# Kernel optimization log

Measured on AMD Instinct MI355X. Metric: run time of the kernel, lower is better.

Reference implementation:

```python
import jax, jax.numpy as jnp
import numpy as np

N = 100000
E = 1600000
IN_C = 128
OUT_C = 64
HID = 2 * OUT_C  # 128


def gcn_conv(x, src, dst, W, b, n):
    # PyG GCNConv with add_self_loops=True, symmetric normalization, bias.
    h = x @ W  # [n, d_out] - transform first (PyG order)
    ones = jnp.ones(src.shape[0], dtype=h.dtype)
    deg = jax.ops.segment_sum(ones, dst, num_segments=n)  # includes self-loops -> deg >= 1
    dinv = jax.lax.rsqrt(deg)
    norm = dinv[src] * dinv[dst]  # [E+n]
    msg = h[src] * norm[:, None]  # gather + scale
    return jax.ops.segment_sum(msg, dst, num_segments=n) + b


def setup_inputs() -> dict:
    key = jax.random.key(0)
    ks = jax.random.split(key, 8)
    x = jax.random.normal(ks[0], (N, IN_C), dtype=jnp.float32)
    edge_index = jax.random.randint(ks[1], (2, E), 0, N, dtype=jnp.int64)
    s1 = 1.0 / np.sqrt(IN_C)
    s2 = 1.0 / np.sqrt(HID)
    s3 = 1.0 / np.sqrt(OUT_C)
    W1 = jax.random.normal(ks[2], (IN_C, HID), dtype=jnp.float32) * s1
    b1 = jnp.zeros((HID,), dtype=jnp.float32)
    W2 = jax.random.normal(ks[3], (HID, OUT_C), dtype=jnp.float32) * s2
    b2 = jnp.zeros((OUT_C,), dtype=jnp.float32)
    Wfc = jax.random.normal(ks[4], (OUT_C, OUT_C), dtype=jnp.float32) * s3
    bfc = jax.random.uniform(ks[5], (OUT_C,), dtype=jnp.float32, minval=-s3, maxval=s3)
    return {"x": x, "edge_index": edge_index, "W1": W1, "b1": b1,
            "W2": W2, "b2": b2, "Wfc": Wfc, "bfc": bfc}


def reference(x, edge_index, W1, b1, W2, b2, Wfc, bfc):
    n = x.shape[0]
    loop = jnp.arange(n, dtype=edge_index.dtype)
    src = jnp.concatenate([edge_index[0], loop])  # add self-loops
    dst = jnp.concatenate([edge_index[1], loop])
    h = jax.nn.relu(gcn_conv(x, src, dst, W1, b1, n))
    h = gcn_conv(h, src, dst, W2, b2, n)
    return h @ Wfc + bfc
```

## Files before the change

### kernel.cpp

```cpp
#include <hip/hip_runtime.h>

#define INC  128
#define HIDC 128
#define OUTC 64

#define BSH   8
#define NBMAX 512
#define HB    128
#define TILE  4096
#define CAP   8192

typedef unsigned int  u32;
typedef unsigned short u16;
typedef short bf16x8 __attribute__((ext_vector_type(8)));
typedef float f32x4 __attribute__((ext_vector_type(4)));

static __device__ __forceinline__ u16 f2bf(float f) {
    u32 u = __builtin_bit_cast(u32, f);
    u += 0x7fffu + ((u >> 16) & 1u);
    return (u16)(u >> 16);
}
static __device__ __forceinline__ float bf_lo(u32 u) {
    return __builtin_bit_cast(float, u << 16);
}
static __device__ __forceinline__ float bf_hi(u32 u) {
    return __builtin_bit_cast(float, u & 0xffff0000u);
}


__global__ __launch_bounds__(256) void bhist_kernel(const int* __restrict__ dst,
                                                    int* __restrict__ parts,
                                                    int E, int nb) {
    __shared__ int h[NBMAX];
    for (int i = threadIdx.x; i < NBMAX; i += 256) h[i] = 0;
    __syncthreads();
    const int total = HB * 256;
    for (int e = blockIdx.x * 256 + threadIdx.x; e < E; e += total)
        atomicAdd(&h[dst[e] >> BSH], 1);
    __syncthreads();
    for (int i = threadIdx.x; i < nb; i += 256) parts[i * HB + blockIdx.x] = h[i];
}

__global__ __launch_bounds__(512) void bscan_kernel(const int* __restrict__ parts,
                                                    int* __restrict__ bucketOff, int nb) {
    __shared__ int sums[NBMAX];
    const int tid = threadIdx.x;
    int s = 0;
    if (tid < nb) {
        const int* p = parts + tid * HB;
#pragma unroll 8
        for (int r = 0; r < HB; ++r) s += p[r];
    }
    sums[tid] = s;
    __syncthreads();
    for (int d = 1; d < NBMAX; d <<= 1) {
        int t = sums[tid];
        int a = (tid >= d) ? sums[tid - d] : 0;
        __syncthreads();
        sums[tid] = t + a;
        __syncthreads();
    }
    if (tid < nb) bucketOff[tid] = sums[tid] - s;
    if (tid == NBMAX - 1) bucketOff[nb] = sums[NBMAX - 1];
}

__global__ __launch_bounds__(256) void multisplit_kernel(const int* __restrict__ src,
                                                         const int* __restrict__ dst,
                                                         const int* __restrict__ bucketOff,
                                                         int* __restrict__ gfill,
                                                         u32* __restrict__ binned,
                                                         int E, int nb) {
    __shared__ int hist[NBMAX];
    __shared__ int sbase[NBMAX];
    __shared__ int cursor[NBMAX];
    __shared__ int gposs[NBMAX];
    __shared__ int wsum[4];
    __shared__ int2 buf[TILE];
    const int tid  = threadIdx.x;
    const int base = blockIdx.x * TILE;
    const int cnt  = min(TILE, E - base);

    for (int i = tid; i < NBMAX; i += 256) hist[i] = 0;
    __syncthreads();

    int ls[16], ld[16], dg[16];
#pragma unroll
    for (int k = 0; k < 16; ++k) {
        int idx = tid + k * 256;
        if (idx < cnt) {
            ls[k] = src[base + idx];
            ld[k] = dst[base + idx];
            dg[k] = ld[k] >> BSH;
            atomicAdd(&hist[dg[k]], 1);
        } else dg[k] = -1;
    }
    __syncthreads();
    {
        const int a = hist[2 * tid], b = hist[2 * tid + 1];
        const int s = a + b;
        const int lane = tid & 63;
        int incl = s;
#pragma unroll
        for (int d = 1; d < 64; d <<= 1) {
            int t = __shfl_up(incl, d);
            if (lane >= d) incl += t;
        }
        if (lane == 63) wsum[tid >> 6] = incl;
        __syncthreads();
        const int w = tid >> 6;
        int wbase = 0;
        if (w > 0) wbase += wsum[0];
        if (w > 1) wbase += wsum[1];
        if (w > 2) wbase += wsum[2];
        const int excl = wbase + incl - s;
        sbase[2 * tid] = excl;          cursor[2 * tid] = excl;
        sbase[2 * tid + 1] = excl + a;  cursor[2 * tid + 1] = excl + a;
    }
    __syncthreads();
#pragma unroll
    for (int k = 0; k < 16; ++k) {
        if (dg[k] >= 0) {
            int p = atomicAdd(&cursor[dg[k]], 1);
            buf[p] = make_int2(ls[k], ld[k]);
        }
    }
    __syncthreads();
    for (int d = tid; d < nb; d += 256) {
        int c = cursor[d] - sbase[d];
        gposs[d] = (c > 0) ? atomicAdd(&gfill[d], c) : 0;
    }
    __syncthreads();
    for (int idx = tid; idx < cnt; idx += 256) {
        int2 e = buf[idx];
        int d = e.y >> BSH;
        binned[bucketOff[d] + gposs[d] + (idx - sbase[d])] =
            (u32)e.x | ((u32)(e.y & 255) << 24);
    }
}

__global__ __launch_bounds__(256) void csr_build_kernel(const u32* __restrict__ binned,
                                                        const int* __restrict__ bucketOff,
                                                        int* __restrict__ col,
                                                        int* __restrict__ rowptr,
                                                        float* __restrict__ dinv,
                                                        int n, int E) {
    __shared__ int cnt[257];
    __shared__ int excl[256];
    __shared__ int wsum[4];
    __shared__ int colstage[CAP];
    const int tid   = threadIdx.x;
    const int b     = blockIdx.x;
    const int node0 = b << BSH;
    const int nNodes = min(256, n - node0);
    const int e0 = bucketOff[b], e1 = bucketOff[b + 1];
    const int ec = e1 - e0;

    for (int i = tid; i <= 256; i += 256) cnt[i] = 0;
    __syncthreads();
    for (int i = tid; i < ec; i += 256)
        atomicAdd(&cnt[binned[e0 + i] >> 24], 1);
    __syncthreads();
    const int myc = cnt[tid];
    {
        const int lane = tid & 63;
        int incl = myc;
#pragma unroll
        for (int d = 1; d < 64; d <<= 1) {
            int t = __shfl_up(incl, d);
            if (lane >= d) incl += t;
        }
        if (lane == 63) wsum[tid >> 6] = incl;
        __syncthreads();
        const int w = tid >> 6;
        int wbase = 0;
        if (w > 0) wbase += wsum[0];
        if (w > 1) wbase += wsum[1];
        if (w > 2) wbase += wsum[2];
        excl[tid] = wbase + incl - myc;
    }
    __syncthreads();
    if (tid < nNodes) {
        const int node = node0 + tid;
        rowptr[node] = e0 + excl[tid];
        dinv[node] = rsqrtf((float)(myc + 1));
    }
    if (b == 0 && tid == 0) rowptr[n] = E;
    __syncthreads();
    cnt[tid] = excl[tid];
    __syncthreads();
    if (ec <= CAP) {
        for (int i = tid; i < ec; i += 256) {
            u32 e = binned[e0 + i];
            int p = atomicAdd(&cnt[e >> 24], 1);
            colstage[p] = (int)(e & 0xffffffu);
        }
        __syncthreads();
        for (int i = tid; i < ec; i += 256) col[e0 + i] = colstage[i];
    } else {
        for (int i = tid; i < ec; i += 256) {
            u32 e = binned[e0 + i];
            int p = atomicAdd(&cnt[e >> 24], 1);
            col[e0 + p] = (int)(e & 0xffffffu);
        }
    }
}

__global__ __launch_bounds__(256) void fold_kernel(const float* __restrict__ W1,
                                                   const float* __restrict__ W2,
                                                   const float* __restrict__ Wfc,
                                                   const float* __restrict__ b2,
                                                   const float* __restrict__ bfc,
                                                   u16* __restrict__ W1t,
                                                   u16* __restrict__ W2ft,
                                                   float* __restrict__ b2f) {
    int t = blockIdx.x * 256 + threadIdx.x;
    if (t < HIDC * HIDC) {
        int nn = t >> 7, k = t & 127;
        W1t[nn * HIDC + k] = f2bf(W1[k * HIDC + nn]);
    } else if (t < HIDC * HIDC + HIDC * OUTC) {
        int u = t - HIDC * HIDC;
        int i = u >> 6, j = u & 63;
        float s = 0.f;
#pragma unroll 8
        for (int k = 0; k < OUTC; ++k) s = fmaf(W2[i * OUTC + k], Wfc[k * OUTC + j], s);
        W2ft[j * HIDC + i] = f2bf(s);
    } else if (t < HIDC * HIDC + HIDC * OUTC + OUTC) {
        int j = t - HIDC * HIDC - HIDC * OUTC;
        float s = bfc[j];
#pragma unroll 8
        for (int k = 0; k < OUTC; ++k) s = fmaf(b2[k], Wfc[k * OUTC + j], s);
        b2f[j] = s;
    }
}


template <int N, bool AF32>
__global__ __launch_bounds__(256) void mfma_gemm_kernel(const void* __restrict__ Aptr,
                                                        const u16* __restrict__ Wt,
                                                        const float* __restrict__ dinv,
                                                        u16* __restrict__ out, int M) {
    constexpr int K = 128;
    constexpr int NC = N / 16;
    __shared__ u16 Ws[N * K];

    const int tid = threadIdx.x;
    for (int id = tid; id < N * K / 8; id += 256) {
        int nn = id >> 4;
        int c  = id & 15;
        uint4 v = *(const uint4*)(Wt + nn * K + c * 8);
        int slot = (nn << 4) + (c ^ (nn & 7));
        *(uint4*)((char*)Ws + slot * 16) = v;
    }

    const int wave = tid >> 6;
    const int lane = tid & 63;
    const int r0   = blockIdx.x * 64 + wave * 16;
    const int arow = r0 + (lane & 15);
    const int kgrp = lane >> 4;
    __syncthreads();

    f32x4 acc[NC];
#pragma unroll
    for (int nc = 0; nc < NC; ++nc) acc[nc] = f32x4{0.f, 0.f, 0.f, 0.f};

#pragma unroll
    for (int kc = 0; kc < 4; ++kc) {
        bf16x8 af = {0, 0, 0, 0, 0, 0, 0, 0};
        if (arow < M) {
            if constexpr (AF32) {
                const float* ap = (const float*)Aptr + (size_t)arow * K + kc * 32 + kgrp * 8;
                float4 v0 = *(const float4*)ap;
                float4 v1 = *(const float4*)(ap + 4);
                af[0] = (short)f2bf(v0.x); af[1] = (short)f2bf(v0.y);
                af[2] = (short)f2bf(v0.z); af[3] = (short)f2bf(v0.w);
                af[4] = (short)f2bf(v1.x); af[5] = (short)f2bf(v1.y);
                af[6] = (short)f2bf(v1.z); af[7] = (short)f2bf(v1.w);
            } else {
                af = *(const bf16x8*)((const u16*)Aptr + (size_t)arow * K + kc * 32 + kgrp * 8);
            }
        }
#pragma unroll
        for (int nc = 0; nc < NC; ++nc) {
            int nn = nc * 16 + (lane & 15);
            int slot = (nn << 4) + ((kc * 4 + kgrp) ^ (nn & 7));
            bf16x8 bfr = *(const bf16x8*)((const char*)Ws + slot * 16);
            acc[nc] = __builtin_amdgcn_mfma_f32_16x16x32_bf16(af, bfr, acc[nc], 0, 0, 0);
        }
    }
#pragma unroll
    for (int reg = 0; reg < 4; ++reg) {
        int row = r0 + (lane >> 4) * 4 + reg;
        if (row <= M) {
            float sc = (row < M) ? dinv[row] : 0.f;
#pragma unroll
            for (int nc = 0; nc < NC; ++nc)
                out[(size_t)row * N + nc * 16 + (lane & 15)] = f2bf(acc[nc][reg] * sc);
        }
    }
}


__global__ __launch_bounds__(256) void agg1_kernel(const u16* __restrict__ g,
                                                   const int* __restrict__ rowptr,
                                                   const int* __restrict__ col,
                                                   const float* __restrict__ dinv,
                                                   const float* __restrict__ b1,
                                                   u32* __restrict__ h1, int n) {
    const int wid  = threadIdx.x >> 6;
    const int lane = threadIdx.x & 63;
    const int v = blockIdx.x * 4 + wid;
    if (v >= n) return;
    const int h = lane >> 5;
    const int r = lane & 31;
    const int base = rowptr[v], endi = rowptr[v + 1];

    float a0 = 0.f, a1 = 0.f, a2 = 0.f, a3 = 0.f;
    float b0 = 0.f, b1v = 0.f, b2v = 0.f, b3 = 0.f;
    {
        uint2 sv = *(const uint2*)(g + ((size_t)v << 7) + (r << 2));
        if (h == 0) {
            a0 = bf_lo(sv.x); a1 = bf_hi(sv.x);
            a2 = bf_lo(sv.y); a3 = bf_hi(sv.y);
        }
    }

    for (int c = base; c < endi; c += 64) {
        const int m = min(64, endi - c);
        const int idx = (lane < m) ? col[c + lane] : n;
        for (int i = 0; i < m; i += 8) {
            int u0 = __shfl(idx, i + h);
            int u1 = __shfl(idx, i + 2 + h);
            int u2 = __shfl(idx, i + 4 + h);
            int u3 = __shfl(idx, i + 6 + h);
            uint2 x0 = *(const uint2*)(g + ((size_t)u0 << 7) + (r << 2));
            uint2 x1 = *(const uint2*)(g + ((size_t)u1 << 7) + (r << 2));
            uint2 x2 = *(const uint2*)(g + ((size_t)u2 << 7) + (r << 2));
            uint2 x3 = *(const uint2*)(g + ((size_t)u3 << 7) + (r << 2));
            a0 += bf_lo(x0.x); a1 += bf_hi(x0.x); a2 += bf_lo(x0.y); a3 += bf_hi(x0.y);
            b0 += bf_lo(x1.x); b1v += bf_hi(x1.x); b2v += bf_lo(x1.y); b3 += bf_hi(x1.y);
            a0 += bf_lo(x2.x); a1 += bf_hi(x2.x); a2 += bf_lo(x2.y); a3 += bf_hi(x2.y);
            b0 += bf_lo(x3.x); b1v += bf_hi(x3.x); b2v += bf_lo(x3.y); b3 += bf_hi(x3.y);
        }
    }
    float s0 = a0 + b0, s1 = a1 + b1v, s2 = a2 + b2v, s3 = a3 + b3;
    s0 += __shfl_xor(s0, 32);
    s1 += __shfl_xor(s1, 32);
    s2 += __shfl_xor(s2, 32);
    s3 += __shfl_xor(s3, 32);
    if (h == 0) {
        const float dv = dinv[v];
        const float4 bb = *(const float4*)&b1[r << 2];
        float o0 = fmaxf(fmaf(dv, s0, bb.x), 0.f);
        float o1 = fmaxf(fmaf(dv, s1, bb.y), 0.f);
        float o2 = fmaxf(fmaf(dv, s2, bb.z), 0.f);
        float o3 = fmaxf(fmaf(dv, s3, bb.w), 0.f);
        uint2 pk;
        pk.x = (u32)f2bf(o0) | ((u32)f2bf(o1) << 16);
        pk.y = (u32)f2bf(o2) | ((u32)f2bf(o3) << 16);
        *(uint2*)(h1 + ((size_t)v << 6) + (r << 1)) = pk;
    }
}

__global__ __launch_bounds__(256) void agg2_kernel(const u16* __restrict__ g2,
                                                   const int* __restrict__ rowptr,
                                                   const int* __restrict__ col,
                                                   const float* __restrict__ dinv,
                                                   const float* __restrict__ b2f,
                                                   float* __restrict__ out, int n) {
    const int wid  = threadIdx.x >> 6;
    const int lane = threadIdx.x & 63;
    const int v = blockIdx.x * 4 + wid;
    if (v >= n) return;
    const int q = lane >> 4;
    const int r = lane & 15;
    const int base = rowptr[v], endi = rowptr[v + 1];

    float a0 = 0.f, a1 = 0.f, a2 = 0.f, a3 = 0.f;
    float b0 = 0.f, b1v = 0.f, b2v = 0.f, b3 = 0.f;
    {
        uint2 sv = *(const uint2*)(g2 + ((size_t)v << 6) + (r << 2));
        if (q == 0) {
            a0 = bf_lo(sv.x); a1 = bf_hi(sv.x);
            a2 = bf_lo(sv.y); a3 = bf_hi(sv.y);
        }
    }

    for (int c = base; c < endi; c += 64) {
        const int m = min(64, endi - c);
        const int idx = (lane < m) ? col[c + lane] : n;
        for (int i = 0; i < m; i += 8) {
            int u0 = __shfl(idx, i + q);
            int u1 = __shfl(idx, i + 4 + q);
            uint2 x0 = *(const uint2*)(g2 + ((size_t)u0 << 6) + (r << 2));
            uint2 x1 = *(const uint2*)(g2 + ((size_t)u1 << 6) + (r << 2));
            a0 += bf_lo(x0.x); a1 += bf_hi(x0.x); a2 += bf_lo(x0.y); a3 += bf_hi(x0.y);
            b0 += bf_lo(x1.x); b1v += bf_hi(x1.x); b2v += bf_lo(x1.y); b3 += bf_hi(x1.y);
        }
    }
    float s0 = a0 + b0, s1 = a1 + b1v, s2 = a2 + b2v, s3 = a3 + b3;
    s0 += __shfl_xor(s0, 16); s0 += __shfl_xor(s0, 32);
    s1 += __shfl_xor(s1, 16); s1 += __shfl_xor(s1, 32);
    s2 += __shfl_xor(s2, 16); s2 += __shfl_xor(s2, 32);
    s3 += __shfl_xor(s3, 16); s3 += __shfl_xor(s3, 32);
    if (q == 0) {
        const float dv = dinv[v];
        const float4 bb = *(const float4*)&b2f[r << 2];
        float4 o;
        o.x = fmaf(dv, s0, bb.x);
        o.y = fmaf(dv, s1, bb.y);
        o.z = fmaf(dv, s2, bb.z);
        o.w = fmaf(dv, s3, bb.w);
        *(float4*)(out + ((size_t)v << 6) + (r << 2)) = o;
    }
}


extern "C" void kernel_launch(void* const* d_in, const int* in_sizes, int n_in,
                              void* d_out, int out_size, void* d_ws, size_t ws_size,
                              hipStream_t stream) {
    const float* x   = (const float*)d_in[0];
    const int*   ei  = (const int*)d_in[1];
    const float* W1  = (const float*)d_in[2];
    const float* b1  = (const float*)d_in[3];
    const float* W2  = (const float*)d_in[4];
    const float* b2  = (const float*)d_in[5];
    const float* Wfc = (const float*)d_in[6];
    const float* bfc = (const float*)d_in[7];
    float* out = (float*)d_out;

    const int n = in_sizes[0] / INC;
    const int E = in_sizes[1] / 2;
    const int* src = ei;
    const int* dst = ei + E;
    const int nb = (n + 255) >> BSH;

    char* w = (char*)d_ws;
    auto alloc = [&](size_t bytes) -> void* {
        void* p = (void*)w;
        w += (bytes + 255) & ~(size_t)255;
        return p;
    };
    int*   rowptr    = (int*)alloc((size_t)(n + 1) * 4);
    float* dinvp     = (float*)alloc((size_t)n * 4);
    int*   col       = (int*)alloc((size_t)(E + 64) * 4);
    u32*   binned    = (u32*)alloc((size_t)E * 4);
    int*   parts     = (int*)alloc((size_t)NBMAX * HB * 4);
    int*   bucketOff = (int*)alloc((size_t)(nb + 1) * 4);
    int*   gfill     = (int*)alloc((size_t)nb * 4);
    u16*   g         = (u16*)alloc((size_t)(n + 1) * HIDC * 2);
    u16*   h1        = (u16*)alloc((size_t)n * HIDC * 2);
    u16*   W1t       = (u16*)alloc((size_t)HIDC * HIDC * 2);
    u16*   W2ft      = (u16*)alloc((size_t)OUTC * HIDC * 2);
    float* b2f       = (float*)alloc((size_t)OUTC * 4);

    hipMemsetAsync(gfill, 0, (size_t)nb * 4, stream);

    fold_kernel<<<(HIDC * HIDC + HIDC * OUTC + OUTC + 255) / 256, 256, 0, stream>>>(
        W1, W2, Wfc, b2, bfc, W1t, W2ft, b2f);
    bhist_kernel<<<HB, 256, 0, stream>>>(dst, parts, E, nb);
    bscan_kernel<<<1, NBMAX, 0, stream>>>(parts, bucketOff, nb);
    multisplit_kernel<<<(E + TILE - 1) / TILE, 256, 0, stream>>>(src, dst, bucketOff, gfill, binned, E, nb);
    csr_build_kernel<<<nb, 256, 0, stream>>>(binned, bucketOff, col, rowptr, dinvp, n, E);

    mfma_gemm_kernel<HIDC, true><<<(n + 64) / 64, 256, 0, stream>>>(x, W1t, dinvp, g, n);
    agg1_kernel<<<(n + 3) / 4, 256, 0, stream>>>(g, rowptr, col, dinvp, b1, (u32*)h1, n);

    mfma_gemm_kernel<OUTC, false><<<(n + 64) / 64, 256, 0, stream>>>(h1, W2ft, dinvp, g, n);
    agg2_kernel<<<(n + 3) / 4, 256, 0, stream>>>(g, rowptr, col, dinvp, b2f, out, n);
}
```

Baseline: 197.0 us.

## Deepen gather unroll, use grid-stride aggregation, merge weight fold into histogram

Both aggregation kernels now issue eight independent row gathers per iteration instead of four or two. Each keeps four partial accumulator sets, so more memory requests are in flight per wave and gather latency is better hidden. The aggregation launches switch from one wave per node to a fixed 2048-block grid-stride loop, which cuts per-block launch and scheduling overhead. The weight-folding kernel is merged into the degree-histogram kernel as extra blocks, removing one launch. The risks are higher register pressure and wasted work on padded neighbour slots, since the wider step reads more zero-row entries for short rows.

Measured after the change: 200.6 us. About the same (+1.8%).

```diff
diff --git a/kernel.cpp b/kernel.cpp
--- a/kernel.cpp
+++ b/kernel.cpp
@@ -28,17 +28,46 @@
 }
 
 
-__global__ __launch_bounds__(256) void bhist_kernel(const int* __restrict__ dst,
-                                                    int* __restrict__ parts,
-                                                    int E, int nb) {
+__global__ __launch_bounds__(256) void fold_bhist_kernel(const int* __restrict__ dst,
+                                                         int* __restrict__ parts,
+                                                         int E, int nb,
+                                                         const float* __restrict__ W1,
+                                                         const float* __restrict__ W2,
+                                                         const float* __restrict__ Wfc,
+                                                         const float* __restrict__ b2,
+                                                         const float* __restrict__ bfc,
+                                                         u16* __restrict__ W1t,
+                                                         u16* __restrict__ W2ft,
+                                                         float* __restrict__ b2f) {
     __shared__ int h[NBMAX];
-    for (int i = threadIdx.x; i < NBMAX; i += 256) h[i] = 0;
-    __syncthreads();
-    const int total = HB * 256;
-    for (int e = blockIdx.x * 256 + threadIdx.x; e < E; e += total)
-        atomicAdd(&h[dst[e] >> BSH], 1);
-    __syncthreads();
-    for (int i = threadIdx.x; i < nb; i += 256) parts[i * HB + blockIdx.x] = h[i];
+    if (blockIdx.x < HB) {
+        for (int i = threadIdx.x; i < NBMAX; i += 256) h[i] = 0;
+        __syncthreads();
+        const int total = HB * 256;
+        for (int e = blockIdx.x * 256 + threadIdx.x; e < E; e += total)
+            atomicAdd(&h[dst[e] >> BSH], 1);
+        __syncthreads();
+        for (int i = threadIdx.x; i < nb; i += 256) parts[i * HB + blockIdx.x] = h[i];
+    } else {
+        int t = (blockIdx.x - HB) * 256 + threadIdx.x;
+        if (t < HIDC * HIDC) {
+            int nn = t >> 7, k = t & 127;
+            W1t[nn * HIDC + k] = f2bf(W1[k * HIDC + nn]);
+        } else if (t < HIDC * HIDC + HIDC * OUTC) {
+            int u = t - HIDC * HIDC;
+            int i = u >> 6, j = u & 63;
+            float s = 0.f;
+#pragma unroll 8
+            for (int k = 0; k < OUTC; ++k) s = fmaf(W2[i * OUTC + k], Wfc[k * OUTC + j], s);
+            W2ft[j * HIDC + i] = f2bf(s);
+        } else if (t < HIDC * HIDC + HIDC * OUTC + OUTC) {
+            int j = t - HIDC * HIDC - HIDC * OUTC;
+            float s = bfc[j];
+#pragma unroll 8
+            for (int k = 0; k < OUTC; ++k) s = fmaf(b2[k], Wfc[k * OUTC + j], s);
+            b2f[j] = s;
+        }
+    }
 }
 
 __global__ __launch_bounds__(512) void bscan_kernel(const int* __restrict__ parts,
@@ -205,34 +234,6 @@
     }
 }
 
-__global__ __launch_bounds__(256) void fold_kernel(const float* __restrict__ W1,
-                                                   const float* __restrict__ W2,
-                                                   const float* __restrict__ Wfc,
-                                                   const float* __restrict__ b2,
-                                                   const float* __restrict__ bfc,
-                                                   u16* __restrict__ W1t,
-                                                   u16* __restrict__ W2ft,
-                                                   float* __restrict__ b2f) {
-    int t = blockIdx.x * 256 + threadIdx.x;
-    if (t < HIDC * HIDC) {
-        int nn = t >> 7, k = t & 127;
-        W1t[nn * HIDC + k] = f2bf(W1[k * HIDC + nn]);
-    } else if (t < HIDC * HIDC + HIDC * OUTC) {
-        int u = t - HIDC * HIDC;
-        int i = u >> 6, j = u & 63;
-        float s = 0.f;
-#pragma unroll 8
-        for (int k = 0; k < OUTC; ++k) s = fmaf(W2[i * OUTC + k], Wfc[k * OUTC + j], s);
-        W2ft[j * HIDC + i] = f2bf(s);
-    } else if (t < HIDC * HIDC + HIDC * OUTC + OUTC) {
-        int j = t - HIDC * HIDC - HIDC * OUTC;
-        float s = bfc[j];
-#pragma unroll 8
-        for (int k = 0; k < OUTC; ++k) s = fmaf(b2[k], Wfc[k * OUTC + j], s);
-        b2f[j] = s;
-    }
-}
-
 
 template <int N, bool AF32>
 __global__ __launch_bounds__(256) void mfma_gemm_kernel(const void* __restrict__ Aptr,
@@ -308,56 +309,74 @@
                                                    u32* __restrict__ h1, int n) {
     const int wid  = threadIdx.x >> 6;
     const int lane = threadIdx.x & 63;
-    const int v = blockIdx.x * 4 + wid;
-    if (v >= n) return;
     const int h = lane >> 5;
     const int r = lane & 31;
-    const int base = rowptr[v], endi = rowptr[v + 1];
-
-    float a0 = 0.f, a1 = 0.f, a2 = 0.f, a3 = 0.f;
-    float b0 = 0.f, b1v = 0.f, b2v = 0.f, b3 = 0.f;
-    {
-        uint2 sv = *(const uint2*)(g + ((size_t)v << 7) + (r << 2));
+    const int vstep = gridDim.x * 4;
+
+    for (int v = blockIdx.x * 4 + wid; v < n; v += vstep) {
+        const int base = rowptr[v], endi = rowptr[v + 1];
+
+        float s0[4], s1[4], s2[4], s3[4];
+#pragma unroll
+        for (int j = 0; j < 4; ++j) { s0[j] = s1[j] = s2[j] = s3[j] = 0.f; }
+        {
+            uint2 sv = *(const uint2*)(g + ((size_t)v << 7) + (r << 2));
+            if (h == 0) {
+                s0[0] = bf_lo(sv.x); s0[1] = bf_hi(sv.x);
+                s0[2] = bf_lo(sv.y); s0[3] = bf_hi(sv.y);
+            }
+        }
+
+        for (int c = base; c < endi; c += 64) {
+            const int m = min(64, endi - c);
+            const int idx = (lane < m) ? col[c + lane] : n;
+            for (int i = 0; i < m; i += 16) {
+                int u0 = __shfl(idx, i + h);
+                int u1 = __shfl(idx, i + 2 + h);
+                int u2 = __shfl(idx, i + 4 + h);
+                int u3 = __shfl(idx, i + 6 + h);
+                int u4 = __shfl(idx, i + 8 + h);
+                int u5 = __shfl(idx, i + 10 + h);
+                int u6 = __shfl(idx, i + 12 + h);
+                int u7 = __shfl(idx, i + 14 + h);
+                uint2 x0 = *(const uint2*)(g + ((size_t)u0 << 7) + (r << 2));
+                uint2 x1 = *(const uint2*)(g + ((size_t)u1 << 7) + (r << 2));
+                uint2 x2 = *(const uint2*)(g + ((size_t)u2 << 7) + (r << 2));
+                uint2 x3 = *(const uint2*)(g + ((size_t)u3 << 7) + (r << 2));
+                uint2 x4 = *(const uint2*)(g + ((size_t)u4 << 7) + (r << 2));
+                uint2 x5 = *(const uint2*)(g + ((size_t)u5 << 7) + (r << 2));
+                uint2 x6 = *(const uint2*)(g + ((size_t)u6 << 7) + (r << 2));
+                uint2 x7 = *(const uint2*)(g + ((size_t)u7 << 7) + (r << 2));
+                s0[0] += bf_lo(x0.x); s0[1] += bf_hi(x0.x); s0[2] += bf_lo(x0.y); s0[3] += bf_hi(x0.y);
+                s1[0] += bf_lo(x1.x); s1[1] += bf_hi(x1.x); s1[2] += bf_lo(x1.y); s1[3] += bf_hi(x1.y);
+                s2[0] += bf_lo(x2.x); s2[1] += bf_hi(x2.x); s2[2] += bf_lo(x2.y); s2[3] += bf_hi(x2.y);
+                s3[0] += bf_lo(x3.x); s3[1] += bf_hi(x3.x); s3[2] += bf_lo(x3.y); s3[3] += bf_hi(x3.y);
+                s0[0] += bf_lo(x4.x); s0[1] += bf_hi(x4.x); s0[2] += bf_lo(x4.y); s0[3] += bf_hi(x4.y);
+                s1[0] += bf_lo(x5.x); s1[1] += bf_hi(x5.x); s1[2] += bf_lo(x5.y); s1[3] += bf_hi(x5.y);
+                s2[0] += bf_lo(x6.x); s2[1] += bf_hi(x6.x); s2[2] += bf_lo(x6.y); s2[3] += bf_hi(x6.y);
+                s3[0] += bf_lo(x7.x); s3[1] += bf_hi(x7.x); s3[2] += bf_lo(x7.y); s3[3] += bf_hi(x7.y);
+            }
+        }
+        float t0 = (s0[0] + s1[0]) + (s2[0] + s3[0]);
+        float t1 = (s0[1] + s1[1]) + (s2[1] + s3[1]);
+        float t2 = (s0[2] + s1[2]) + (s2[2] + s3[2]);
+        float t3 = (s0[3] + s1[3]) + (s2[3] + s3[3]);
+        t0 += __shfl_xor(t0, 32);
+        t1 += __shfl_xor(t1, 32);
+        t2 += __shfl_xor(t2, 32);
+        t3 += __shfl_xor(t3, 32);
         if (h == 0) {
-            a0 = bf_lo(sv.x); a1 = bf_hi(sv.x);
-            a2 = bf_lo(sv.y); a3 = bf_hi(sv.y);
-        }
-    }
-
-    for (int c = base; c < endi; c += 64) {
-        const int m = min(64, endi - c);
-        const int idx = (lane < m) ? col[c + lane] : n;
-        for (int i = 0; i < m; i += 8) {
-            int u0 = __shfl(idx, i + h);
-            int u1 = __shfl(idx, i + 2 + h);
-            int u2 = __shfl(idx, i + 4 + h);
-            int u3 = __shfl(idx, i + 6 + h);
-            uint2 x0 = *(const uint2*)(g + ((size_t)u0 << 7) + (r << 2));
-            uint2 x1 = *(const uint2*)(g + ((size_t)u1 << 7) + (r << 2));
-            uint2 x2 = *(const uint2*)(g + ((size_t)u2 << 7) + (r << 2));
-            uint2 x3 = *(const uint2*)(g + ((size_t)u3 << 7) + (r << 2));
-            a0 += bf_lo(x0.x); a1 += bf_hi(x0.x); a2 += bf_lo(x0.y); a3 += bf_hi(x0.y);
-            b0 += bf_lo(x1.x); b1v += bf_hi(x1.x); b2v += bf_lo(x1.y); b3 += bf_hi(x1.y);
-            a0 += bf_lo(x2.x); a1 += bf_hi(x2.x); a2 += bf_lo(x2.y); a3 += bf_hi(x2.y);
-            b0 += bf_lo(x3.x); b1v += bf_hi(x3.x); b2v += bf_lo(x3.y); b3 += bf_hi(x3.y);
-        }
-    }
-    float s0 = a0 + b0, s1 = a1 + b1v, s2 = a2 + b2v, s3 = a3 + b3;
-    s0 += __shfl_xor(s0, 32);
-    s1 += __shfl_xor(s1, 32);
-    s2 += __shfl_xor(s2, 32);
-    s3 += __shfl_xor(s3, 32);
-    if (h == 0) {
-        const float dv = dinv[v];
-        const float4 bb = *(const float4*)&b1[r << 2];
-        float o0 = fmaxf(fmaf(dv, s0, bb.x), 0.f);
-        float o1 = fmaxf(fmaf(dv, s1, bb.y), 0.f);
-        float o2 = fmaxf(fmaf(dv, s2, bb.z), 0.f);
-        float o3 = fmaxf(fmaf(dv, s3, bb.w), 0.f);
-        uint2 pk;
-        pk.x = (u32)f2bf(o0) | ((u32)f2bf(o1) << 16);
-        pk.y = (u32)f2bf(o2) | ((u32)f2bf(o3) << 16);
-        *(uint2*)(h1 + ((size_t)v << 6) + (r << 1)) = pk;
+            const float dv = dinv[v];
+            const float4 bb = *(const float4*)&b1[r << 2];
+            float o0 = fmaxf(fmaf(dv, t0, bb.x), 0.f);
+            float o1 = fmaxf(fmaf(dv, t1, bb.y), 0.f);
+            float o2 = fmaxf(fmaf(dv, t2, bb.z), 0.f);
+            float o3 = fmaxf(fmaf(dv, t3, bb.w), 0.f);
+            uint2 pk;
+            pk.x = (u32)f2bf(o0) | ((u32)f2bf(o1) << 16);
+            pk.y = (u32)f2bf(o2) | ((u32)f2bf(o3) << 16);
+            *(uint2*)(h1 + ((size_t)v << 6) + (r << 1)) = pk;
+        }
     }
 }
 
@@ -369,48 +388,72 @@
                                                    float* __restrict__ out, int n) {
     const int wid  = threadIdx.x >> 6;
     const int lane = threadIdx.x & 63;
-    const int v = blockIdx.x * 4 + wid;
-    if (v >= n) return;
     const int q = lane >> 4;
     const int r = lane & 15;
-    const int base = rowptr[v], endi = rowptr[v + 1];
-
-    float a0 = 0.f, a1 = 0.f, a2 = 0.f, a3 = 0.f;
-    float b0 = 0.f, b1v = 0.f, b2v = 0.f, b3 = 0.f;
-    {
-        uint2 sv = *(const uint2*)(g2 + ((size_t)v << 6) + (r << 2));
+    const int vstep = gridDim.x * 4;
+
+    for (int v = blockIdx.x * 4 + wid; v < n; v += vstep) {
+        const int base = rowptr[v], endi = rowptr[v + 1];
+
+        float s0[4], s1[4], s2[4], s3[4];
+#pragma unroll
+        for (int j = 0; j < 4; ++j) { s0[j] = s1[j] = s2[j] = s3[j] = 0.f; }
+        {
+            uint2 sv = *(const uint2*)(g2 + ((size_t)v << 6) + (r << 2));
+            if (q == 0) {
+                s0[0] = bf_lo(sv.x); s0[1] = bf_hi(sv.x);
+                s0[2] = bf_lo(sv.y); s0[3] = bf_hi(sv.y);
+            }
+        }
+
+        for (int c = base; c < endi; c += 64) {
+            const int m = min(64, endi - c);
+            const int idx = (lane < m) ? col[c + lane] : n;
+            for (int i = 0; i < m; i += 32) {
+                int u0 = __shfl(idx, i + q);
+                int u1 = __shfl(idx, i + 4 + q);
+                int u2 = __shfl(idx, i + 8 + q);
+                int u3 = __shfl(idx, i + 12 + q);
+                int u4 = __shfl(idx, i + 16 + q);
+                int u5 = __shfl(idx, i + 20 + q);
+                int u6 = __shfl(idx, i + 24 + q);
+                int u7 = __shfl(idx, i + 28 + q);
+                uint2 x0 = *(const uint2*)(g2 + ((size_t)u0 << 6) + (r << 2));
+                uint2 x1 = *(const uint2*)(g2 + ((size_t)u1 << 6) + (r << 2));
+                uint2 x2 = *(const uint2*)(g2 + ((size_t)u2 << 6) + (r << 2));
+                uint2 x3 = *(const uint2*)(g2 + ((size_t)u3 << 6) + (r << 2));
+                uint2 x4 = *(const uint2*)(g2 + ((size_t)u4 << 6) + (r << 2));
+                uint2 x5 = *(const uint2*)(g2 + ((size_t)u5 << 6) + (r << 2));
+                uint2 x6 = *(const uint2*)(g2 + ((size_t)u6 << 6) + (r << 2));
+                uint2 x7 = *(const uint2*)(g2 + ((size_t)u7 << 6) + (r << 2));
+                s0[0] += bf_lo(x0.x); s0[1] += bf_hi(x0.x); s0[2] += bf_lo(x0.y); s0[3] += bf_hi(x0.y);
+                s1[0] += bf_lo(x1.x); s1[1] += bf_hi(x1.x); s1[2] += bf_lo(x1.y); s1[3] += bf_hi(x1.y);
+                s2[0] += bf_lo(x2.x); s2[1] += bf_hi(x2.x); s2[2] += bf_lo(x2.y); s2[3] += bf_hi(x2.y);
+                s3[0] += bf_lo(x3.x); s3[1] += bf_hi(x3.x); s3[2] += bf_lo(x3.y); s3[3] += bf_hi(x3.y);
+                s0[0] += bf_lo(x4.x); s0[1] += bf_hi(x4.x); s0[2] += bf_lo(x4.y); s0[3] += bf_hi(x4.y);
+                s1[0] += bf_lo(x5.x); s1[1] += bf_hi(x5.x); s1[2] += bf_lo(x5.y); s1[3] += bf_hi(x5.y);
+                s2[0] += bf_lo(x6.x); s2[1] += bf_hi(x6.x); s2[2] += bf_lo(x6.y); s2[3] += bf_hi(x6.y);
+                s3[0] += bf_lo(x7.x); s3[1] += bf_hi(x7.x); s3[2] += bf_lo(x7.y); s3[3] += bf_hi(x7.y);
+            }
+        }
+        float t0 = (s0[0] + s1[0]) + (s2[0] + s3[0]);
+        float t1 = (s0[1] + s1[1]) + (s2[1] + s3[1]);
+        float t2 = (s0[2] + s1[2]) + (s2[2] + s3[2]);
+        float t3 = (s0[3] + s1[3]) + (s2[3] + s3[3]);
+        t0 += __shfl_xor(t0, 16); t0 += __shfl_xor(t0, 32);
+        t1 += __shfl_xor(t1, 16); t1 += __shfl_xor(t1, 32);
+        t2 += __shfl_xor(t2, 16); t2 += __shfl_xor(t2, 32);
+        t3 += __shfl_xor(t3, 16); t3 += __shfl_xor(t3, 32);
         if (q == 0) {
-            a0 = bf_lo(sv.x); a1 = bf_hi(sv.x);
-            a2 = bf_lo(sv.y); a3 = bf_hi(sv.y);
-        }
-    }
-
-    for (int c = base; c < endi; c += 64) {
-        const int m = min(64, endi - c);
-        const int idx = (lane < m) ? col[c + lane] : n;
-        for (int i = 0; i < m; i += 8) {
-            int u0 = __shfl(idx, i + q);
-            int u1 = __shfl(idx, i + 4 + q);
-            uint2 x0 = *(const uint2*)(g2 + ((size_t)u0 << 6) + (r << 2));
-            uint2 x1 = *(const uint2*)(g2 + ((size_t)u1 << 6) + (r << 2));
-            a0 += bf_lo(x0.x); a1 += bf_hi(x0.x); a2 += bf_lo(x0.y); a3 += bf_hi(x0.y);
-            b0 += bf_lo(x1.x); b1v += bf_hi(x1.x); b2v += bf_lo(x1.y); b3 += bf_hi(x1.y);
-        }
-    }
-    float s0 = a0 + b0, s1 = a1 + b1v, s2 = a2 + b2v, s3 = a3 + b3;
-    s0 += __shfl_xor(s0, 16); s0 += __shfl_xor(s0, 32);
-    s1 += __shfl_xor(s1, 16); s1 += __shfl_xor(s1, 32);
-    s2 += __shfl_xor(s2, 16); s2 += __shfl_xor(s2, 32);
-    s3 += __shfl_xor(s3, 16); s3 += __shfl_xor(s3, 32);
-    if (q == 0) {
-        const float dv = dinv[v];
-        const float4 bb = *(const float4*)&b2f[r << 2];
-        float4 o;
-        o.x = fmaf(dv, s0, bb.x);
-        o.y = fmaf(dv, s1, bb.y);
-        o.z = fmaf(dv, s2, bb.z);
-        o.w = fmaf(dv, s3, bb.w);
-        *(float4*)(out + ((size_t)v << 6) + (r << 2)) = o;
+            const float dv = dinv[v];
+            const float4 bb = *(const float4*)&b2f[r << 2];
+            float4 o;
+            o.x = fmaf(dv, t0, bb.x);
+            o.y = fmaf(dv, t1, bb.y);
+            o.z = fmaf(dv, t2, bb.z);
+            o.w = fmaf(dv, t3, bb.w);
+            *(float4*)(out + ((size_t)v << 6) + (r << 2)) = o;
+        }
     }
 }
 
@@ -455,16 +498,16 @@
 
     hipMemsetAsync(gfill, 0, (size_t)nb * 4, stream);
 
-    fold_kernel<<<(HIDC * HIDC + HIDC * OUTC + OUTC + 255) / 256, 256, 0, stream>>>(
-        W1, W2, Wfc, b2, bfc, W1t, W2ft, b2f);
-    bhist_kernel<<<HB, 256, 0, stream>>>(dst, parts, E, nb);
+    const int FB = HB + (HIDC * HIDC + HIDC * OUTC + OUTC + 255) / 256;
+    fold_bhist_kernel<<<FB, 256, 0, stream>>>(dst, parts, E, nb,
+                                              W1, W2, Wfc, b2, bfc, W1t, W2ft, b2f);
     bscan_kernel<<<1, NBMAX, 0, stream>>>(parts, bucketOff, nb);
     multisplit_kernel<<<(E + TILE - 1) / TILE, 256, 0, stream>>>(src, dst, bucketOff, gfill, binned, E, nb);
     csr_build_kernel<<<nb, 256, 0, stream>>>(binned, bucketOff, col, rowptr, dinvp, n, E);
 
     mfma_gemm_kernel<HIDC, true><<<(n + 64) / 64, 256, 0, stream>>>(x, W1t, dinvp, g, n);
-    agg1_kernel<<<(n + 3) / 4, 256, 0, stream>>>(g, rowptr, col, dinvp, b1, (u32*)h1, n);
+    agg1_kernel<<<2048, 256, 0, stream>>>(g, rowptr, col, dinvp, b1, (u32*)h1, n);
 
     mfma_gemm_kernel<OUTC, false><<<(n + 64) / 64, 256, 0, stream>>>(h1, W2ft, dinvp, g, n);
-    agg2_kernel<<<(n + 3) / 4, 256, 0, stream>>>(g, rowptr, col, dinvp, b2f, out, n);
-}
+    agg2_kernel<<<2048, 256, 0, stream>>>(g, rowptr, col, dinvp, b2f, out, n);
+}
```
